# Kernel optimization log

Measured on AMD Instinct MI355X. Metric: run time of the kernel, lower is better.

## Reference

```python
import jax, jax.numpy as jnp
import numpy as np

N_DRUG = 20000
N_TARGET = 20000
N = N_DRUG + N_TARGET
E = 500000
D = 128
L = 2
NEG_SLOPE = 0.2


def _gat(h, edge_index, W, asrc, adst, edge_bias=None):
    """Single-head GAT layer: h [N,d] -> [N,d]."""
    n = h.shape[0]
    hp = h @ W                                   # [N,d]
    src, dst = edge_index[0], edge_index[1]      # [E]
    logit = (hp @ asrc)[src] + (hp @ adst)[dst]  # [E]
    if edge_bias is not None:
        logit = logit + edge_bias
    e = jax.nn.leaky_relu(logit, NEG_SLOPE)
    # numerically-stable softmax over incoming edges of each dst node
    m = jax.ops.segment_max(e, dst, num_segments=n)
    m = jnp.where(jnp.isfinite(m), m, 0.0)
    ex = jnp.exp(e - m[dst])                     # [E]
    denom = jax.ops.segment_sum(ex, dst, num_segments=n) + 1e-16  # [N]
    num = jax.ops.segment_sum(ex[:, None] * hp[src], dst, num_segments=n)  # [N,d]
    return jax.nn.elu(num / denom[:, None])


def _forward(x_drug, x_target, W_drug, b_drug, W_target, b_target,
             W_gat, a_src, a_dst, a_edge, edge_attr_dd,
             edge_dd, edge_dt, edge_tt):
    h = jnp.concatenate([x_drug @ W_drug + b_drug,
                         x_target @ W_target + b_target], axis=0)  # [N,d]
    for l in range(L):
        bias_dd = edge_attr_dd @ a_edge[l]  # [E] additive attention bias
        x1 = _gat(h, edge_dd, W_gat[l, 0], a_src[l, 0], a_dst[l, 0], bias_dd)
        x2 = _gat(h, edge_dt, W_gat[l, 1], a_src[l, 1], a_dst[l, 1])
        x3 = _gat(h, edge_tt, W_gat[l, 2], a_src[l, 2], a_dst[l, 2])
        h = (x1 + x2 + x3) / 3.0
    return h


def setup_inputs() -> dict:
    key = jax.random.key(0)
    ks = jax.random.split(key, 16)
    s_in = lambda f: 1.0 / np.sqrt(f)
    edge_dd = jax.random.randint(ks[0], (2, E), 0, N_DRUG, dtype=jnp.int32)
    edge_tt = jax.random.randint(ks[1], (2, E), N_DRUG, N, dtype=jnp.int32)
    dt_src = jax.random.randint(ks[2], (E,), 0, N_DRUG, dtype=jnp.int32)
    dt_dst = jax.random.randint(ks[3], (E,), N_DRUG, N, dtype=jnp.int32)
    edge_dt = jnp.stack([dt_src, dt_dst], axis=0)
    return {
        "x_drug": jax.random.normal(ks[4], (N_DRUG, 2048), jnp.float32),
        "x_target": jax.random.normal(ks[5], (N_TARGET, 1280), jnp.float32),
        "W_drug": jax.random.normal(ks[6], (2048, D), jnp.float32) * s_in(2048),
        "b_drug": jnp.zeros((D,), jnp.float32),
        "W_target": jax.random.normal(ks[7], (1280, D), jnp.float32) * s_in(1280),
        "b_target": jnp.zeros((D,), jnp.float32),
        "W_gat": jax.random.normal(ks[8], (L, 3, D, D), jnp.float32) * s_in(D),
        "a_src": jax.random.normal(ks[9], (L, 3, D), jnp.float32) * s_in(D),
        "a_dst": jax.random.normal(ks[10], (L, 3, D), jnp.float32) * s_in(D),
        "a_edge": jax.random.normal(ks[11], (L, D), jnp.float32) * s_in(D),
        "edge_attr_dd": jax.random.normal(ks[12], (E, D), jnp.float32),
        "edge_dd": edge_dd,
        "edge_dt": edge_dt,
        "edge_tt": edge_tt,
    }


def reference(x_drug, x_target, W_drug, b_drug, W_target, b_target,
              W_gat, a_src, a_dst, a_edge, edge_attr_dd,
              edge_dd, edge_dt, edge_tt):
    h = _forward(x_drug, x_target, W_drug, b_drug, W_target, b_target,
                 W_gat, a_src, a_dst, a_edge, edge_attr_dd,
                 edge_dd, edge_dt, edge_tt)
    return h[:N_DRUG], h[N_DRUG:]
```

## Files before the change

### kernel.cpp

```cpp
#include <hip/hip_runtime.h>
#include <hip/hip_fp16.h>
#include <hip/hip_bf16.h>

#define NDRUG 20000
#define NTGT  20000
#define NN    40000
#define NE    500000
#define DDIM  128
#define CAP   96
#define NB    313
#define AS1 __attribute__((address_space(1)))
#define AS3 __attribute__((address_space(3)))

typedef __attribute__((ext_vector_type(4))) float f32x4;
typedef __attribute__((ext_vector_type(8))) short s16x8;
typedef __attribute__((ext_vector_type(4))) unsigned u32x4;

__device__ inline unsigned short bf_rn(float x) {
  unsigned u = __float_as_uint(x);
  return (unsigned short)((u + 0x7FFFu + ((u >> 16) & 1u)) >> 16);
}
__device__ __forceinline__ void split1(float x, short& h, short& l) {
  const unsigned u = __float_as_uint(x);
  const unsigned hu = (u + 0x7FFFu + ((u >> 16) & 1u)) & 0xFFFF0000u;
  h = (short)(hu >> 16);
  l = (short)bf_rn(x - __uint_as_float(hu));
}
__device__ __forceinline__ void split_pk(float x0, float x1, unsigned& hp, unsigned& lp) {
  __hip_bfloat162 h2 = __float22bfloat162_rn(make_float2(x0, x1));
  unsigned hu; __builtin_memcpy(&hu, &h2, 4);
  const float f0 = __uint_as_float(hu << 16);
  const float f1 = __uint_as_float(hu & 0xFFFF0000u);
  __hip_bfloat162 l2 = __float22bfloat162_rn(make_float2(x0 - f0, x1 - f1));
  unsigned lu; __builtin_memcpy(&lu, &l2, 4);
  hp = hu; lp = lu;
}
__device__ __forceinline__ void cvt8_pk(const float4 a, const float4 b, s16x8& h, s16x8& l) {
  unsigned h0, h1, h2, h3, l0, l1, l2, l3;
  split_pk(a.x, a.y, h0, l0);
  split_pk(a.z, a.w, h1, l1);
  split_pk(b.x, b.y, h2, l2);
  split_pk(b.z, b.w, h3, l3);
  u32x4 hu = {h0, h1, h2, h3};
  u32x4 lu = {l0, l1, l2, l3};
  h = __builtin_bit_cast(s16x8, hu);
  l = __builtin_bit_cast(s16x8, lu);
}
__device__ __forceinline__ void glds16(const void* g, void* l) {
  __builtin_amdgcn_global_load_lds((const AS1 unsigned*)g, (AS3 unsigned*)l, 16, 0, 0);
}
__device__ __forceinline__ f32x4 mfma(const s16x8& a, const s16x8& b, const f32x4& c) {
  return __builtin_amdgcn_mfma_f32_16x16x32_bf16(a, b, c, 0, 0, 0);
}
__device__ __forceinline__ int swz(int c) { return c ^ ((c >> 3) & 7); }

__global__ void prep_pack(const float* __restrict__ W, short* __restrict__ ph,
                          short* __restrict__ pl, int K) {
  const size_t mat = (size_t)blockIdx.y * K * 128;
  const int idx = blockIdx.x * blockDim.x + threadIdx.x;
  if (idx >= K * 128) return;
  const int kt = idx >> 12, r = idx & 4095;
  const int dchunk = r >> 3, j = r & 7;
  const int c = swz(dchunk);
  const int col = c >> 2, kg = c & 3;
  const int k = kt * 32 + kg * 8 + j;
  short h, l;
  split1(W[mat + (size_t)k * 128 + col], h, l);
  ph[mat + idx] = h;
  pl[mat + idx] = l;
}

__global__ __launch_bounds__(256)
void gemm_proj(const float* __restrict__ xd, const short* __restrict__ pdh,
               const short* __restrict__ pdl, const float* __restrict__ bd,
               const float* __restrict__ xt, const short* __restrict__ pth,
               const short* __restrict__ ptl, const float* __restrict__ bt,
               short* __restrict__ hh, short* __restrict__ hl) {
  __shared__ float Af[2][64 * 32];
  __shared__ short Bf[2][2][4096];

  int b = blockIdx.x;
  const float* A; const short* BH; const short* BL; const float* bias;
  int M, K, rowbase;
  if (b < 313) { A = xd; BH = pdh; BL = pdl; bias = bd; M = NDRUG; K = 2048; rowbase = 0; }
  else { b -= 313; A = xt; BH = pth; BL = ptl; bias = bt; M = NTGT; K = 1280; rowbase = NDRUG; }
  const int bm = b * 64;
  const int t = threadIdx.x, w = t >> 6, lane = t & 63;
  const int lr = lane & 15, kg = lane >> 4;
  const int steps = K >> 5;

  const int ad0 = (w << 6) + lane, ad1 = ad0 + 256;
  const int ar0 = ad0 >> 3, ar1 = ad1 >> 3;
  const int ac0 = (ad0 & 7) ^ (ar0 & 7), ac1 = (ad1 & 7) ^ (ar1 & 7);
  int gr0 = bm + ar0; if (gr0 >= M) gr0 = M - 1;
  int gr1 = bm + ar1; if (gr1 >= M) gr1 = M - 1;
  const float* asrc0 = A + (size_t)gr0 * K + ac0 * 4;
  const float* asrc1 = A + (size_t)gr1 * K + ac1 * 4;
  const int bd0 = (w << 6) + lane, bd1 = bd0 + 256;

  f32x4 acc[8] = {};

  auto stage = [&](int buf, int kt) {
    const int kk = kt << 5;
    glds16(asrc0 + kk, &Af[buf][(w << 6) * 4]);
    glds16(asrc1 + kk, &Af[buf][(256 + (w << 6)) * 4]);
    const size_t bo = (size_t)kt * 4096;
    glds16(BH + bo + bd0 * 8, &Bf[buf][0][(w << 6) * 8]);
    glds16(BH + bo + bd1 * 8, &Bf[buf][0][(256 + (w << 6)) * 8]);
    glds16(BL + bo + bd0 * 8, &Bf[buf][1][(w << 6) * 8]);
    glds16(BL + bo + bd1 * 8, &Bf[buf][1][(256 + (w << 6)) * 8]);
  };

  const int arow = (w << 4) + lr;
  const int ap0 = (arow * 8 + ((kg * 2) ^ (arow & 7))) * 4;
  const int ap1 = (arow * 8 + ((kg * 2 + 1) ^ (arow & 7))) * 4;

  auto compute = [&](int buf) {
    const float4 va = *(const float4*)&Af[buf][ap0];
    const float4 vb = *(const float4*)&Af[buf][ap1];
    s16x8 ah, al;
    cvt8_pk(va, vb, ah, al);
#pragma unroll
    for (int n = 0; n < 8; ++n) {
      const int c = ((n * 16 + lr) << 2) + kg;
      const int pos = swz(c) << 3;
      const s16x8 bh = *(const s16x8*)&Bf[buf][0][pos];
      const s16x8 bl = *(const s16x8*)&Bf[buf][1][pos];
      acc[n] = mfma(ah, bh, acc[n]);
      acc[n] = mfma(ah, bl, acc[n]);
      acc[n] = mfma(al, bh, acc[n]);
    }
  };

  stage(0, 0);
  __syncthreads();
  int cur = 0;
  for (int kt = 0; kt < steps - 1; ++kt) {
    stage(cur ^ 1, kt + 1);
    compute(cur);
    __syncthreads();
    cur ^= 1;
  }
  compute(cur);

#pragma unroll
  for (int n = 0; n < 8; ++n) {
    const int col = n * 16 + lr;
    const float bv = bias[col];
#pragma unroll
    for (int r = 0; r < 4; ++r) {
      const int row = bm + (w << 4) + kg * 4 + r;
      if (row < M) {
        short h, l;
        split1(acc[n][r] + bv, h, l);
        hh[(size_t)(rowbase + row) * DDIM + col] = h;
        hl[(size_t)(rowbase + row) * DDIM + col] = l;
      }
    }
  }
}

__global__ __launch_bounds__(256)
void gemm_gat(const short* __restrict__ ahh, const short* __restrict__ ahl,
              const short* __restrict__ PH3, const short* __restrict__ PL3,
              const float* __restrict__ asrc3, const float* __restrict__ adst3,
              __half* __restrict__ hp16, float* __restrict__ s_all,
              float* __restrict__ d_all) {
  __shared__ short Apl[2][2][2048];
  __shared__ short Bf[2][2][4096];

  const int rel = blockIdx.y;
  const int bm = blockIdx.x * 64;
  const short* BH = PH3 + (size_t)rel * DDIM * DDIM;
  const short* BL = PL3 + (size_t)rel * DDIM * DDIM;
  const int t = threadIdx.x, w = t >> 6, lane = t & 63;
  const int lr = lane & 15, kg = lane >> 4;

  const int apn = w >> 1;
  const short* aplane = apn ? ahl : ahh;
  const int ad0 = ((w & 1) << 6) + lane, ad1 = ad0 + 128;
  const int ac0 = swz(ad0), ac1 = swz(ad1);
  const short* asrc0 = aplane + (size_t)(bm + (ac0 >> 2)) * DDIM + (ac0 & 3) * 8;
  const short* asrc1 = aplane + (size_t)(bm + (ac1 >> 2)) * DDIM + (ac1 & 3) * 8;
  const int bd0 = (w << 6) + lane, bd1 = bd0 + 256;

  f32x4 acc[8] = {};

  auto stage = [&](int buf, int kt) {
    const int kk = kt << 5;
    glds16(asrc0 + kk, &Apl[buf][apn][ad0 * 8]);
    glds16(asrc1 + kk, &Apl[buf][apn][ad1 * 8]);
    const size_t bo = (size_t)kt * 4096;
    glds16(BH + bo + bd0 * 8, &Bf[buf][0][(w << 6) * 8]);
    glds16(BH + bo + bd1 * 8, &Bf[buf][0][(256 + (w << 6)) * 8]);
    glds16(BL + bo + bd0 * 8, &Bf[buf][1][(w << 6) * 8]);
    glds16(BL + bo + bd1 * 8, &Bf[buf][1][(256 + (w << 6)) * 8]);
  };

  const int arow = (w << 4) + lr;
  const int apos = swz((arow << 2) + kg) << 3;

  auto compute = [&](int buf) {
    const s16x8 ah = *(const s16x8*)&Apl[buf][0][apos];
    const s16x8 al = *(const s16x8*)&Apl[buf][1][apos];
#pragma unroll
    for (int n = 0; n < 8; ++n) {
      const int c = ((n * 16 + lr) << 2) + kg;
      const int pos = swz(c) << 3;
      const s16x8 bh = *(const s16x8*)&Bf[buf][0][pos];
      const s16x8 bl = *(const s16x8*)&Bf[buf][1][pos];
      acc[n] = mfma(ah, bh, acc[n]);
      acc[n] = mfma(ah, bl, acc[n]);
      acc[n] = mfma(al, bh, acc[n]);
    }
  };

  stage(0, 0);
  __syncthreads();
  int cur = 0;
  for (int kt = 0; kt < 3; ++kt) {
    stage(cur ^ 1, kt + 1);
    compute(cur);
    __syncthreads();
    cur ^= 1;
  }
  compute(cur);

  __half* hpr = hp16 + (size_t)rel * NN * DDIM;
  float asv[8], adv[8];
#pragma unroll
  for (int n = 0; n < 8; ++n) {
    asv[n] = asrc3[rel * DDIM + n * 16 + lr];
    adv[n] = adst3[rel * DDIM + n * 16 + lr];
  }
#pragma unroll
  for (int r = 0; r < 4; ++r) {
    const int row = bm + (w << 4) + kg * 4 + r;
    float ps = 0.f, pd = 0.f;
#pragma unroll
    for (int n = 0; n < 8; ++n) {
      hpr[(size_t)row * DDIM + n * 16 + lr] = __float2half_rn(acc[n][r]);
      ps += acc[n][r] * asv[n];
      pd += acc[n][r] * adv[n];
    }
#pragma unroll
    for (int o = 1; o < 16; o <<= 1) { ps += __shfl_xor(ps, o); pd += __shfl_xor(pd, o); }
    if (lr == 0) {
      s_all[(size_t)rel * NN + row] = ps;
      d_all[(size_t)rel * NN + row] = pd;
    }
  }
}

__global__ __launch_bounds__(256)
void edge_bias_kernel(const float* __restrict__ ea, const float* __restrict__ ae0,
                      const float* __restrict__ ae1, float* __restrict__ b0,
                      float* __restrict__ b1) {
  const int wave = threadIdx.x >> 6, lane = threadIdx.x & 63;
  const int e = blockIdx.x * 4 + wave;
  if (e >= NE) return;
  const float2 v = *(const float2*)(ea + (size_t)e * DDIM + (lane << 1));
  float s0 = v.x * ae0[lane << 1] + v.y * ae0[(lane << 1) + 1];
  float s1 = v.x * ae1[lane << 1] + v.y * ae1[(lane << 1) + 1];
#pragma unroll
  for (int o = 32; o; o >>= 1) { s0 += __shfl_xor(s0, o); s1 += __shfl_xor(s1, o); }
  if (lane == 0) { b0[e] = s0; b1[e] = s1; }
}


__global__ __launch_bounds__(256)
void hist3(const int* __restrict__ d0, const int* __restrict__ d1,
           const int* __restrict__ d2, int* __restrict__ bcnt) {
  __shared__ int h[NB];
  const int rel = blockIdx.y;
  const int* dst = rel == 0 ? d0 : (rel == 1 ? d1 : d2);
  const int t = threadIdx.x;
  for (int i = t; i < NB; i += 256) h[i] = 0;
  __syncthreads();
  for (int e = blockIdx.x * 256 + t; e < NE; e += gridDim.x * 256)
    atomicAdd(&h[dst[e] >> 7], 1);
  __syncthreads();
  for (int i = t; i < NB; i += 256)
    if (h[i]) atomicAdd(&bcnt[rel * NB + i], h[i]);
}

__global__ __launch_bounds__(1024)
void scanb(const int* __restrict__ bcnt, int* __restrict__ bbase,
           int* __restrict__ bcur, int* __restrict__ offs_all) {
  __shared__ int part[1024];
  const int t = threadIdx.x;
  const int v = (t < 3 * NB) ? bcnt[t] : 0;
  part[t] = v;
  __syncthreads();
  for (int o = 1; o < 1024; o <<= 1) {
    const int pv = (t >= o) ? part[t - o] : 0;
    __syncthreads();
    part[t] += pv;
    __syncthreads();
  }
  if (t < 3 * NB) {
    const int excl = part[t] - v;
    const int base = excl - (t / NB) * NE;
    bbase[t] = base;
    bcur[t] = base;
  }
  if (t < 3) offs_all[t * (NN + 1) + NN] = NE;
}

#define BIN_BLK 64
__global__ __launch_bounds__(256)
void bin3(const int* __restrict__ s0, const int* __restrict__ d0,
          const int* __restrict__ s1, const int* __restrict__ d1,
          const int* __restrict__ s2, const int* __restrict__ d2,
          int* __restrict__ bcur, int2* __restrict__ binned) {
  __shared__ int lhist[NB], lbase[NB];
  const int rel = blockIdx.y;
  const int* src = rel == 0 ? s0 : (rel == 1 ? s1 : s2);
  const int* dst = rel == 0 ? d0 : (rel == 1 ? d1 : d2);
  int2* bout = binned + (size_t)rel * NE;
  const int per = (NE + BIN_BLK - 1) / BIN_BLK;
  const int e0 = blockIdx.x * per;
  const int e1 = min(e0 + per, NE);
  const int t = threadIdx.x;
  for (int i = t; i < NB; i += 256) lhist[i] = 0;
  __syncthreads();
  for (int e = e0 + t; e < e1; e += 256) atomicAdd(&lhist[dst[e] >> 7], 1);
  __syncthreads();
  for (int i = t; i < NB; i += 256) {
    const int c = lhist[i];
    lbase[i] = c ? atomicAdd(&bcur[rel * NB + i], c) : 0;
  }
  __syncthreads();
  for (int i = t; i < NB; i += 256) lhist[i] = 0;
  __syncthreads();
  for (int e = e0 + t; e < e1; e += 256) {
    const int d = dst[e];
    const int b = d >> 7;
    const int p = lbase[b] + atomicAdd(&lhist[b], 1);
    bout[p] = make_int2(src[e], (e << 7) | (d & 127));
  }
}

__global__ __launch_bounds__(256)
void csr_bucket(const int2* __restrict__ binned, const int* __restrict__ bbase,
                const int* __restrict__ bcnt, int* __restrict__ offs_all,
                int* __restrict__ csrc_all, int* __restrict__ ceid0) {
  __shared__ int hist[128], scan[128], curs[128];
  const int rel = blockIdx.y, b = blockIdx.x;
  const int base = bbase[rel * NB + b];
  const int n = bcnt[rel * NB + b];
  const int t = threadIdx.x;
  if (t < 128) hist[t] = 0;
  __syncthreads();
  const int2* seg = binned + (size_t)rel * NE + base;
  for (int i = t; i < n; i += 256) atomicAdd(&hist[seg[i].y & 127], 1);
  __syncthreads();
  if (t < 128) scan[t] = hist[t];
  __syncthreads();
  for (int o = 1; o < 128; o <<= 1) {
    const int pv = (t >= o && t < 128) ? scan[t - o] : 0;
    __syncthreads();
    if (t < 128) scan[t] += pv;
    __syncthreads();
  }
  if (t < 128) {
    const int excl = base + scan[t] - hist[t];
    const int node = b * 128 + t;
    if (node < NN) offs_all[rel * (NN + 1) + node] = excl;
    curs[t] = excl;
  }
  __syncthreads();
  int* csrc = csrc_all + (size_t)rel * NE;
  for (int i = t; i < n; i += 256) {
    const int2 v = seg[i];
    const int p = atomicAdd(&curs[v.y & 127], 1);
    csrc[p] = v.x;
    if (rel == 0) ceid0[p] = v.y >> 7;
  }
}

__device__ __forceinline__ void gat_one(const int* __restrict__ offs,
                                        const int* __restrict__ csrc,
                                        const int* __restrict__ ceid,
                                        const float* __restrict__ ebias,
                                        const float* __restrict__ s, float dn,
                                        const __half* __restrict__ hpr, int node,
                                        float* exbuf, int* srcbuf, int lane,
                                        float& o0, float& o1) {
  const int beg = offs[node];
  int cnt = offs[node + 1] - beg;
  if (cnt > CAP) cnt = CAP;
  if (cnt == 0) return;
  __threadfence_block();
  float m = -1e30f;
  for (int i = lane; i < cnt; i += 64) {
    const int sn = csrc[beg + i];
    float logit = s[sn] + dn;
    if (ebias) logit += ebias[ceid[beg + i]];
    const float e = logit >= 0.f ? logit : 0.2f * logit;
    exbuf[i] = e;
    srcbuf[i] = sn;
    m = fmaxf(m, e);
  }
#pragma unroll
  for (int o = 32; o; o >>= 1) m = fmaxf(m, __shfl_xor(m, o));
  float ssum = 0.f;
  for (int i = lane; i < cnt; i += 64) {
    const float ex = __expf(exbuf[i] - m);
    exbuf[i] = ex;
    ssum += ex;
  }
#pragma unroll
  for (int o = 32; o; o >>= 1) ssum += __shfl_xor(ssum, o);
  const float inv = 1.f / (ssum + 1e-16f);
  __threadfence_block();
  const int c = lane << 1;
  float n0 = 0.f, n1 = 0.f;
  int i = 0;
  for (; i + 2 <= cnt; i += 2) {
    const float w0 = exbuf[i], w1 = exbuf[i + 1];
    const float2 v0 = __half22float2(*(const __half2*)(hpr + (size_t)srcbuf[i] * DDIM + c));
    const float2 v1 = __half22float2(*(const __half2*)(hpr + (size_t)srcbuf[i + 1] * DDIM + c));
    n0 += w0 * v0.x + w1 * v1.x;
    n1 += w0 * v0.y + w1 * v1.y;
  }
  for (; i < cnt; ++i) {
    const float w = exbuf[i];
    const float2 v = __half22float2(*(const __half2*)(hpr + (size_t)srcbuf[i] * DDIM + c));
    n0 += w * v.x;
    n1 += w * v.y;
  }
  const float v0 = n0 * inv, v1 = n1 * inv;
  o0 += (v0 > 0.f ? v0 : expm1f(v0));
  o1 += (v1 > 0.f ? v1 : expm1f(v1));
}

__global__ __launch_bounds__(256)
void agg_all(const int* __restrict__ offs_all, const int* __restrict__ csrc_all,
             const int* __restrict__ ceid0, const float* __restrict__ ebias,
             const float* __restrict__ s_all, const float* __restrict__ d_all,
             const __half* __restrict__ hp16, float* __restrict__ outf,
             short* __restrict__ ohh, short* __restrict__ ohl, int write_f32) {
  __shared__ float exbuf[4][CAP];
  __shared__ int   srcbuf[4][CAP];
  const int wave = threadIdx.x >> 6, lane = threadIdx.x & 63;
  const int node = blockIdx.x * 4 + wave;
  float o0 = 0.f, o1 = 0.f;
  if (node < NDRUG) {
    gat_one(offs_all, csrc_all, ceid0, ebias, s_all, d_all[node],
            hp16, node, exbuf[wave], srcbuf[wave], lane, o0, o1);
  } else {
#pragma unroll
    for (int rel = 1; rel <= 2; ++rel) {
      gat_one(offs_all + rel * (NN + 1), csrc_all + (size_t)rel * NE, nullptr, nullptr,
              s_all + (size_t)rel * NN, d_all[(size_t)rel * NN + node],
              hp16 + (size_t)rel * NN * DDIM, node, exbuf[wave], srcbuf[wave], lane, o0, o1);
    }
  }
  o0 *= (1.f / 3.f);
  o1 *= (1.f / 3.f);
  const int c = lane << 1;
  if (write_f32) {
    *(float2*)(outf + (size_t)node * DDIM + c) = make_float2(o0, o1);
  } else {
    short h0, l0, h1, l1;
    split1(o0, h0, l0);
    split1(o1, h1, l1);
    *(short2*)(ohh + (size_t)node * DDIM + c) = make_short2(h0, h1);
    *(short2*)(ohl + (size_t)node * DDIM + c) = make_short2(l0, l1);
  }
}

extern "C" void kernel_launch(void* const* d_in, const int* in_sizes, int n_in,
                              void* d_out, int out_size, void* d_ws, size_t ws_size,
                              hipStream_t stream) {
  const float* x_drug    = (const float*)d_in[0];
  const float* x_target  = (const float*)d_in[1];
  const float* W_drug    = (const float*)d_in[2];
  const float* b_drug    = (const float*)d_in[3];
  const float* W_target  = (const float*)d_in[4];
  const float* b_target  = (const float*)d_in[5];
  const float* W_gat     = (const float*)d_in[6];
  const float* a_src     = (const float*)d_in[7];
  const float* a_dst     = (const float*)d_in[8];
  const float* a_edge    = (const float*)d_in[9];
  const float* edge_attr = (const float*)d_in[10];
  const int*   e_dd      = (const int*)d_in[11];
  const int*   e_dt      = (const int*)d_in[12];
  const int*   e_tt      = (const int*)d_in[13];
  float* out = (float*)d_out;

  char* ws = (char*)d_ws;
  size_t off = 0;
  auto alloc = [&](size_t b) -> void* {
    void* p = ws + off;
    off += (b + 255) & ~(size_t)255;
    return p;
  };
  __half* hp16  = (__half*)alloc((size_t)3 * NN * DDIM * 2);
  short* hhA    = (short*)alloc((size_t)NN * DDIM * 2);
  short* hlA    = (short*)alloc((size_t)NN * DDIM * 2);
  short* hhB    = (short*)alloc((size_t)NN * DDIM * 2);
  short* hlB    = (short*)alloc((size_t)NN * DDIM * 2);
  float* s_all  = (float*)alloc((size_t)3 * NN * 4);
  float* d_allb = (float*)alloc((size_t)3 * NN * 4);
  float* bias0  = (float*)alloc((size_t)NE * 4);
  float* bias1  = (float*)alloc((size_t)NE * 4);
  int* bcnt     = (int*)alloc((size_t)3 * NB * 4);
  int* bbase    = (int*)alloc((size_t)3 * NB * 4);
  int* bcur     = (int*)alloc((size_t)3 * NB * 4);
  int2* binned  = (int2*)alloc((size_t)3 * NE * 8);
  int* offs_all = (int*)alloc((size_t)3 * (NN + 1) * 4);
  int* csrc_all = (int*)alloc((size_t)3 * NE * 4);
  int* ceid0    = (int*)alloc((size_t)NE * 4);
  short* pwd_h  = (short*)alloc((size_t)2048 * 128 * 2);
  short* pwd_l  = (short*)alloc((size_t)2048 * 128 * 2);
  short* pwt_h  = (short*)alloc((size_t)1280 * 128 * 2);
  short* pwt_l  = (short*)alloc((size_t)1280 * 128 * 2);
  short* pwg_h  = (short*)alloc((size_t)6 * 128 * 128 * 2);
  short* pwg_l  = (short*)alloc((size_t)6 * 128 * 128 * 2);

  prep_pack<<<dim3(1024, 1), 256, 0, stream>>>(W_drug, pwd_h, pwd_l, 2048);
  prep_pack<<<dim3(640, 1), 256, 0, stream>>>(W_target, pwt_h, pwt_l, 1280);
  prep_pack<<<dim3(64, 6), 256, 0, stream>>>(W_gat, pwg_h, pwg_l, 128);

  gemm_proj<<<626, 256, 0, stream>>>(x_drug, pwd_h, pwd_l, b_drug,
                                     x_target, pwt_h, pwt_l, b_target, hhA, hlA);

  edge_bias_kernel<<<NE / 4, 256, 0, stream>>>(edge_attr, a_edge, a_edge + DDIM,
                                               bias0, bias1);
  hipMemsetAsync(bcnt, 0, (size_t)3 * NB * 4, stream);
  hist3<<<dim3(64, 3), 256, 0, stream>>>(e_dd + NE, e_dt + NE, e_tt + NE, bcnt);
  scanb<<<1, 1024, 0, stream>>>(bcnt, bbase, bcur, offs_all);
  bin3<<<dim3(BIN_BLK, 3), 256, 0, stream>>>(e_dd, e_dd + NE, e_dt, e_dt + NE,
                                             e_tt, e_tt + NE, bcur, binned);
  csr_bucket<<<dim3(NB, 3), 256, 0, stream>>>(binned, bbase, bcnt, offs_all,
                                              csrc_all, ceid0);

  gemm_gat<<<dim3(625, 3), 256, 0, stream>>>(hhA, hlA, pwg_h, pwg_l,
                                             a_src, a_dst, hp16, s_all, d_allb);
  agg_all<<<NN / 4, 256, 0, stream>>>(offs_all, csrc_all, ceid0, bias0,
                                      s_all, d_allb, hp16, nullptr, hhB, hlB, 0);
  gemm_gat<<<dim3(625, 3), 256, 0, stream>>>(hhB, hlB,
                                             pwg_h + (size_t)3 * DDIM * DDIM,
                                             pwg_l + (size_t)3 * DDIM * DDIM,
                                             a_src + 3 * DDIM, a_dst + 3 * DDIM,
                                             hp16, s_all, d_allb);
  agg_all<<<NN / 4, 256, 0, stream>>>(offs_all, csrc_all, ceid0, bias1,
                                      s_all, d_allb, hp16, out, nullptr, nullptr, 1);
}
```

Baseline: 474.9 us.

## Merge weight-pack kernels and fuse projection GEMM, edge bias, histogram into one launch

Folds the three weight-packing launches into one kernel and merges the input projection GEMM, the edge-attention bias reduction and the destination histogram into a single heterogeneous kernel whose blocks pick their role from the block index. The edge-bias part becomes a grid-stride loop over fewer blocks, with the attention weights loaded once per wave. The goal is to cut launch overhead and let the memory-bound bias and histogram work run alongside the compute-bound GEMM. In exchange, every block reserves the GEMM's 48KB of dynamic shared memory, which can lower occupancy for the light roles.

```diff
diff --git a/kernel.cpp b/kernel.cpp
--- a/kernel.cpp
+++ b/kernel.cpp
@@ -11,6 +11,11 @@
 #define NB    313
 #define AS1 __attribute__((address_space(1)))
 #define AS3 __attribute__((address_space(3)))
+
+#define PROJ_BLK 626
+#define EB_BLK   1024
+#define HIST_BLK 192
+#define FRONT_GRID (PROJ_BLK + EB_BLK + HIST_BLK)
 
 typedef __attribute__((ext_vector_type(4))) float f32x4;
 typedef __attribute__((ext_vector_type(8))) short s16x8;
@@ -54,10 +59,23 @@
 }
 __device__ __forceinline__ int swz(int c) { return c ^ ((c >> 3) & 7); }
 
-__global__ void prep_pack(const float* __restrict__ W, short* __restrict__ ph,
-                          short* __restrict__ pl, int K) {
-  const size_t mat = (size_t)blockIdx.y * K * 128;
-  const int idx = blockIdx.x * blockDim.x + threadIdx.x;
+__global__ void prep_all(const float* __restrict__ Wd, const float* __restrict__ Wt,
+                         const float* __restrict__ Wg, short* __restrict__ pdh,
+                         short* __restrict__ pdl, short* __restrict__ pth,
+                         short* __restrict__ ptl, short* __restrict__ pgh,
+                         short* __restrict__ pgl) {
+  int b = blockIdx.x;
+  const float* W; short* ph; short* pl; int K; int idx;
+  if (b < 1024) { W = Wd; ph = pdh; pl = pdl; K = 2048; idx = b * 256 + threadIdx.x; }
+  else if (b < 1664) { W = Wt; ph = pth; pl = ptl; K = 1280; idx = (b - 1024) * 256 + threadIdx.x; }
+  else {
+    const int bb = b - 1664, mat = bb >> 6;
+    W = Wg + (size_t)mat * 128 * 128;
+    ph = pgh + (size_t)mat * 128 * 128;
+    pl = pgl + (size_t)mat * 128 * 128;
+    K = 128;
+    idx = (bb & 63) * 256 + threadIdx.x;
+  }
   if (idx >= K * 128) return;
   const int kt = idx >> 12, r = idx & 4095;
   const int dchunk = r >> 3, j = r & 7;
@@ -65,19 +83,56 @@
   const int col = c >> 2, kg = c & 3;
   const int k = kt * 32 + kg * 8 + j;
   short h, l;
-  split1(W[mat + (size_t)k * 128 + col], h, l);
-  ph[mat + idx] = h;
-  pl[mat + idx] = l;
+  split1(W[(size_t)k * 128 + col], h, l);
+  ph[idx] = h;
+  pl[idx] = l;
 }
 
 __global__ __launch_bounds__(256)
-void gemm_proj(const float* __restrict__ xd, const short* __restrict__ pdh,
-               const short* __restrict__ pdl, const float* __restrict__ bd,
-               const float* __restrict__ xt, const short* __restrict__ pth,
-               const short* __restrict__ ptl, const float* __restrict__ bt,
-               short* __restrict__ hh, short* __restrict__ hl) {
-  __shared__ float Af[2][64 * 32];
-  __shared__ short Bf[2][2][4096];
+void front(const float* __restrict__ xd, const short* __restrict__ pdh,
+           const short* __restrict__ pdl, const float* __restrict__ bd,
+           const float* __restrict__ xt, const short* __restrict__ pth,
+           const short* __restrict__ ptl, const float* __restrict__ bt,
+           short* __restrict__ hh, short* __restrict__ hl,
+           const float* __restrict__ ea, const float* __restrict__ ae0,
+           const float* __restrict__ ae1, float* __restrict__ eb0,
+           float* __restrict__ eb1,
+           const int* __restrict__ dd_dst, const int* __restrict__ dt_dst,
+           const int* __restrict__ tt_dst, int* __restrict__ bcnt) {
+  extern __shared__ char smem[];
+  const int t = threadIdx.x, w = t >> 6, lane = t & 63;
+
+  if (blockIdx.x >= PROJ_BLK + EB_BLK) {
+    int* h = (int*)smem;
+    const int hb = blockIdx.x - (PROJ_BLK + EB_BLK);
+    const int rel = hb >> 6, blk = hb & 63;
+    const int* dst = rel == 0 ? dd_dst : (rel == 1 ? dt_dst : tt_dst);
+    for (int i = t; i < NB; i += 256) h[i] = 0;
+    __syncthreads();
+    for (int e = blk * 256 + t; e < NE; e += 64 * 256)
+      atomicAdd(&h[dst[e] >> 7], 1);
+    __syncthreads();
+    for (int i = t; i < NB; i += 256)
+      if (h[i]) atomicAdd(&bcnt[rel * NB + i], h[i]);
+    return;
+  }
+  if (blockIdx.x >= PROJ_BLK) {
+    const int wid = (blockIdx.x - PROJ_BLK) * 4 + w;
+    const float a00 = ae0[lane << 1], a01 = ae0[(lane << 1) + 1];
+    const float a10 = ae1[lane << 1], a11 = ae1[(lane << 1) + 1];
+    for (int e = wid; e < NE; e += EB_BLK * 4) {
+      const float2 v = *(const float2*)(ea + (size_t)e * DDIM + (lane << 1));
+      float s0 = v.x * a00 + v.y * a01;
+      float s1 = v.x * a10 + v.y * a11;
+#pragma unroll
+      for (int o = 32; o; o >>= 1) { s0 += __shfl_xor(s0, o); s1 += __shfl_xor(s1, o); }
+      if (lane == 0) { eb0[e] = s0; eb1[e] = s1; }
+    }
+    return;
+  }
+
+  float* Af = (float*)smem;
+  short* Bf = (short*)(smem + 16384);
 
   int b = blockIdx.x;
   const float* A; const short* BH; const short* BL; const float* bias;
@@ -85,7 +140,6 @@
   if (b < 313) { A = xd; BH = pdh; BL = pdl; bias = bd; M = NDRUG; K = 2048; rowbase = 0; }
   else { b -= 313; A = xt; BH = pth; BL = ptl; bias = bt; M = NTGT; K = 1280; rowbase = NDRUG; }
   const int bm = b * 64;
-  const int t = threadIdx.x, w = t >> 6, lane = t & 63;
   const int lr = lane & 15, kg = lane >> 4;
   const int steps = K >> 5;
 
@@ -102,13 +156,15 @@
 
   auto stage = [&](int buf, int kt) {
     const int kk = kt << 5;
-    glds16(asrc0 + kk, &Af[buf][(w << 6) * 4]);
-    glds16(asrc1 + kk, &Af[buf][(256 + (w << 6)) * 4]);
+    glds16(asrc0 + kk, Af + buf * 2048 + (w << 8));
+    glds16(asrc1 + kk, Af + buf * 2048 + 1024 + (w << 8));
     const size_t bo = (size_t)kt * 4096;
-    glds16(BH + bo + bd0 * 8, &Bf[buf][0][(w << 6) * 8]);
-    glds16(BH + bo + bd1 * 8, &Bf[buf][0][(256 + (w << 6)) * 8]);
-    glds16(BL + bo + bd0 * 8, &Bf[buf][1][(w << 6) * 8]);
-    glds16(BL + bo + bd1 * 8, &Bf[buf][1][(256 + (w << 6)) * 8]);
+    short* B0 = Bf + (size_t)(buf * 2 + 0) * 4096;
+    short* B1 = Bf + (size_t)(buf * 2 + 1) * 4096;
+    glds16(BH + bo + bd0 * 8, B0 + (w << 9));
+    glds16(BH + bo + bd1 * 8, B0 + 2048 + (w << 9));
+    glds16(BL + bo + bd0 * 8, B1 + (w << 9));
+    glds16(BL + bo + bd1 * 8, B1 + 2048 + (w << 9));
   };
 
   const int arow = (w << 4) + lr;
@@ -116,16 +172,18 @@
   const int ap1 = (arow * 8 + ((kg * 2 + 1) ^ (arow & 7))) * 4;
 
   auto compute = [&](int buf) {
-    const float4 va = *(const float4*)&Af[buf][ap0];
-    const float4 vb = *(const float4*)&Af[buf][ap1];
+    const float4 va = *(const float4*)(Af + buf * 2048 + ap0);
+    const float4 vb = *(const float4*)(Af + buf * 2048 + ap1);
     s16x8 ah, al;
     cvt8_pk(va, vb, ah, al);
+    const short* B0 = Bf + (size_t)(buf * 2 + 0) * 4096;
+    const short* B1 = Bf + (size_t)(buf * 2 + 1) * 4096;
 #pragma unroll
     for (int n = 0; n < 8; ++n) {
       const int c = ((n * 16 + lr) << 2) + kg;
       const int pos = swz(c) << 3;
-      const s16x8 bh = *(const s16x8*)&Bf[buf][0][pos];
-      const s16x8 bl = *(const s16x8*)&Bf[buf][1][pos];
+      const s16x8 bh = *(const s16x8*)(B0 + pos);
+      const s16x8 bl = *(const s16x8*)(B1 + pos);
       acc[n] = mfma(ah, bh, acc[n]);
       acc[n] = mfma(ah, bl, acc[n]);
       acc[n] = mfma(al, bh, acc[n]);
@@ -250,38 +308,6 @@
       d_all[(size_t)rel * NN + row] = pd;
     }
   }
-}
-
-__global__ __launch_bounds__(256)
-void edge_bias_kernel(const float* __restrict__ ea, const float* __restrict__ ae0,
-                      const float* __restrict__ ae1, float* __restrict__ b0,
-                      float* __restrict__ b1) {
-  const int wave = threadIdx.x >> 6, lane = threadIdx.x & 63;
-  const int e = blockIdx.x * 4 + wave;
-  if (e >= NE) return;
-  const float2 v = *(const float2*)(ea + (size_t)e * DDIM + (lane << 1));
-  float s0 = v.x * ae0[lane << 1] + v.y * ae0[(lane << 1) + 1];
-  float s1 = v.x * ae1[lane << 1] + v.y * ae1[(lane << 1) + 1];
-#pragma unroll
-  for (int o = 32; o; o >>= 1) { s0 += __shfl_xor(s0, o); s1 += __shfl_xor(s1, o); }
-  if (lane == 0) { b0[e] = s0; b1[e] = s1; }
-}
-
-
-__global__ __launch_bounds__(256)
-void hist3(const int* __restrict__ d0, const int* __restrict__ d1,
-           const int* __restrict__ d2, int* __restrict__ bcnt) {
-  __shared__ int h[NB];
-  const int rel = blockIdx.y;
-  const int* dst = rel == 0 ? d0 : (rel == 1 ? d1 : d2);
-  const int t = threadIdx.x;
-  for (int i = t; i < NB; i += 256) h[i] = 0;
-  __syncthreads();
-  for (int e = blockIdx.x * 256 + t; e < NE; e += gridDim.x * 256)
-    atomicAdd(&h[dst[e] >> 7], 1);
-  __syncthreads();
-  for (int i = t; i < NB; i += 256)
-    if (h[i]) atomicAdd(&bcnt[rel * NB + i], h[i]);
 }
 
 __global__ __launch_bounds__(1024)
@@ -520,17 +546,16 @@
   short* pwg_h  = (short*)alloc((size_t)6 * 128 * 128 * 2);
   short* pwg_l  = (short*)alloc((size_t)6 * 128 * 128 * 2);
 
-  prep_pack<<<dim3(1024, 1), 256, 0, stream>>>(W_drug, pwd_h, pwd_l, 2048);
-  prep_pack<<<dim3(640, 1), 256, 0, stream>>>(W_target, pwt_h, pwt_l, 1280);
-  prep_pack<<<dim3(64, 6), 256, 0, stream>>>(W_gat, pwg_h, pwg_l, 128);
-
-  gemm_proj<<<626, 256, 0, stream>>>(x_drug, pwd_h, pwd_l, b_drug,
-                                     x_target, pwt_h, pwt_l, b_target, hhA, hlA);
-
-  edge_bias_kernel<<<NE / 4, 256, 0, stream>>>(edge_attr, a_edge, a_edge + DDIM,
-                                               bias0, bias1);
+  prep_all<<<1024 + 640 + 384, 256, 0, stream>>>(W_drug, W_target, W_gat,
+                                                 pwd_h, pwd_l, pwt_h, pwt_l,
+                                                 pwg_h, pwg_l);
   hipMemsetAsync(bcnt, 0, (size_t)3 * NB * 4, stream);
-  hist3<<<dim3(64, 3), 256, 0, stream>>>(e_dd + NE, e_dt + NE, e_tt + NE, bcnt);
+
+  front<<<FRONT_GRID, 256, 49152, stream>>>(
+      x_drug, pwd_h, pwd_l, b_drug, x_target, pwt_h, pwt_l, b_target, hhA, hlA,
+      edge_attr, a_edge, a_edge + DDIM, bias0, bias1,
+      e_dd + NE, e_dt + NE, e_tt + NE, bcnt);
+
   scanb<<<1, 1024, 0, stream>>>(bcnt, bbase, bcur, offs_all);
   bin3<<<dim3(BIN_BLK, 3), 256, 0, stream>>>(e_dd, e_dd + NE, e_dt, e_dt + NE,
                                              e_tt, e_tt + NE, bcur, binned);
```

After: 511.2 us. +7.6%, slower.
